# Performance work log

Hardware: AMD Instinct MI355X
Metric: run time of the kernel (lower is better)

The kernel has to match this reference:

```python
import jax, jax.numpy as jnp
import numpy as np

N, E = 50000, 800000
D_IN, HID, H = 128, 64, 4
NEG_SLOPE = 0.2

def setup_inputs() -> dict:
    key = jax.random.key(0)
    ks = jax.random.split(key, 12)
    r = lambda i, shape, s=1.0: jax.random.normal(ks[i], shape, jnp.float32) * s
    return dict(
        x=r(0, (N, D_IN)),
        edge_index=jax.random.randint(ks[1], (2, E), 0, N, jnp.int32),
        W_in=r(2, (D_IN, HID), 0.05), b_in=jnp.zeros((HID,), jnp.float32),
        W1=r(3, (D_IN, H * HID), 0.05), a1_src=r(4, (H, HID), 0.05), a1_dst=r(5, (H, HID), 0.05), b1=jnp.zeros((HID,), jnp.float32),
        W2=r(6, (HID, H * HID), 0.05), a2_src=r(7, (H, HID), 0.05), a2_dst=r(8, (H, HID), 0.05), b2=jnp.zeros((HID,), jnp.float32),
        g1=jnp.ones((HID,), jnp.float32), be1=jnp.zeros((HID,), jnp.float32),
        g2=jnp.ones((HID,), jnp.float32), be2=jnp.zeros((HID,), jnp.float32),
        Wo=r(9, (HID, HID), 0.05), bo=jnp.zeros((HID,), jnp.float32),
    )

def layer_norm(x, g, b, eps=1e-5):
    mu = x.mean(-1, keepdims=True)
    var = ((x - mu) ** 2).mean(-1, keepdims=True)
    return (x - mu) * jax.lax.rsqrt(var + eps) * g + b

def gat_conv(x, W, a_src, a_dst, b, src, dst):
    # PyG GATConv, concat=False (mean over heads), self-loops already in src/dst
    n = x.shape[0]
    h = (x @ W).reshape(n, H, HID)                      # [N,H,C]
    e_src = jnp.einsum('nhc,hc->nh', h, a_src)          # [N,H]
    e_dst = jnp.einsum('nhc,hc->nh', h, a_dst)
    e = jax.nn.leaky_relu(e_src[src] + e_dst[dst], NEG_SLOPE)   # [E+N,H]
    # segment softmax over destination nodes
    m = jax.ops.segment_max(e, dst, num_segments=n)
    e = jnp.exp(e - m[dst])
    s = jax.ops.segment_sum(e, dst, num_segments=n)
    alpha = e / (s[dst] + 1e-16)                        # [E+N,H]
    msg = h[src] * alpha[:, :, None]                    # [E+N,H,C]
    out = jax.ops.segment_sum(msg, dst, num_segments=n) # [N,H,C]
    return out.mean(axis=1) + b                         # concat=False -> mean

def reference(x, W_in, b_in, W1, a1_src, a1_dst, b1, W2, a2_src, a2_dst, b2,
              g1, be1, g2, be2, Wo, bo, edge_index):
    loop = jnp.arange(N, dtype=edge_index.dtype)
    src = jnp.concatenate([edge_index[0], loop])
    dst = jnp.concatenate([edge_index[1], loop])
    residual = x @ W_in + b_in
    h = jax.nn.elu(gat_conv(x, W1, a1_src, a1_dst, b1, src, dst))
    h = layer_norm(h + residual, g1, be1)
    h2 = jax.nn.elu(gat_conv(h, W2, a2_src, a2_dst, b2, src, dst))
    h = layer_norm(h2 + h, g2, be2)
    return h @ Wo + bo
```

## Files before the change

### kernel.cpp

```cpp
#include <hip/hip_runtime.h>


using short8 = __attribute__((ext_vector_type(8))) short;
using floatx4 = __attribute__((ext_vector_type(4))) float;
using floatx2 = __attribute__((ext_vector_type(2))) float;

#define OVCAP 65536

__device__ __forceinline__ float wave_sum(float v) {
#pragma unroll
  for (int m = 32; m >= 1; m >>= 1) v += __shfl_xor(v, m, 64);
  return v;
}
__device__ __forceinline__ float wave_max(float v) {
#pragma unroll
  for (int m = 32; m >= 1; m >>= 1) v = fmaxf(v, __shfl_xor(v, m, 64));
  return v;
}
__device__ __forceinline__ unsigned pack_bf16(float lo, float hi) {
  unsigned r;
  asm volatile("v_cvt_pk_bf16_f32 %0, %1, %2" : "=v"(r) : "v"(lo), "v"(hi));
  return r;
}
__device__ __forceinline__ float bf_lo(unsigned u) { return __uint_as_float(u << 16); }
__device__ __forceinline__ float bf_hi(unsigned u) { return __uint_as_float(u & 0xffff0000u); }
__device__ __forceinline__ float lrelu(float e) { return e > 0.f ? e : 0.2f * e; }
__device__ __forceinline__ unsigned pack_fp8x4(float h0, float h1, float h2,
                                               float h3) {
  int u = __builtin_amdgcn_cvt_pk_fp8_f32(h0, h1, 0, false);
  u = __builtin_amdgcn_cvt_pk_fp8_f32(h2, h3, u, true);
  return (unsigned)u;
}

__device__ __forceinline__ void scatter_edge(const int* __restrict__ src,
                                             const int* __restrict__ dst,
                                             int* __restrict__ cnt,
                                             int* __restrict__ srcs,
                                             uint2* __restrict__ ov,
                                             int* __restrict__ ovcnt, int e) {
  int d = dst[e], s = src[e];
  int pos = atomicAdd(&cnt[d], 1);
  if (pos < 63) {
    srcs[(long)d * 64 + pos] = s;
  } else {
    int o = atomicAdd(ovcnt, 1);
    if (o < OVCAP) ov[o] = make_uint2((unsigned)s, (unsigned)d);
  }
}

__device__ __forceinline__ float waDot(const float* W, const float* a, int k,
                                       int h) {
  float s = 0.f;
#pragma unroll 8
  for (int c = 0; c < 64; ++c) s += W[k * 256 + h * 64 + c] * a[h * 64 + c];
  return s;
}
__device__ __forceinline__ void pack_body(
    int t, int l, const float* __restrict__ W1, const float* __restrict__ Win,
    const float* __restrict__ a1s, const float* __restrict__ a1d,
    const float* __restrict__ W2, const float* __restrict__ a2s,
    const float* __restrict__ a2d, const float* __restrict__ Wo,
    ushort* __restrict__ Bpk1, ushort* __restrict__ Bpk2,
    ushort* __restrict__ Bpk3) {
  const int l15 = l & 15, lhi = l >> 4;
  float w[8];
  ushort* dstp;
  if (t < 84) {
    const int kt = t / 21, nt = t - kt * 21;
    const int kb = kt * 32 + lhi * 8, col = nt * 16 + l15;
#pragma unroll
    for (int e = 0; e < 8; ++e) {
      int k = kb + e;
      float v = 0.f;
      if (col < 256) v = W1[k * 256 + col];
      else if (col < 320) v = Win[k * 64 + (col - 256)];
      else if (col < 324) v = waDot(W1, a1s, k, col - 320);
      else if (col < 328) v = waDot(W1, a1d, k, col - 324);
      w[e] = v;
    }
    dstp = Bpk1 + ((long)t * 64 + l) * 8;
  } else if (t < 120) {
    const int t2 = t - 84;
    if (t2 >= 34) return;
    const int kt = t2 / 17, nt = t2 - kt * 17;
    const int kb = kt * 32 + lhi * 8, col = nt * 16 + l15;
#pragma unroll
    for (int e = 0; e < 8; ++e) {
      int k = kb + e;
      float v = 0.f;
      if (col < 256) v = W2[k * 256 + col];
      else if (col < 260) v = waDot(W2, a2s, k, col - 256);
      else if (col < 264) v = waDot(W2, a2d, k, col - 260);
      w[e] = v;
    }
    dstp = Bpk2 + ((long)t2 * 64 + l) * 8;
  } else {
    const int t3 = t - 120;
    if (t3 >= 8) return;
    const int kt = t3 / 4, nt = t3 - kt * 4;
    const int kb = kt * 32 + lhi * 8, col = nt * 16 + l15;
#pragma unroll
    for (int e = 0; e < 8; ++e) w[e] = Wo[(kb + e) * 64 + col];
    dstp = Bpk3 + ((long)t3 * 64 + l) * 8;
  }
  uint4 o;
  o.x = pack_bf16(w[0], w[1]);
  o.y = pack_bf16(w[2], w[3]);
  o.z = pack_bf16(w[4], w[5]);
  o.w = pack_bf16(w[6], w[7]);
  *(uint4*)dstp = o;
}

template <int KA, int KT, int NT, int MODE>
__device__ __forceinline__ void gemm_body(
    const float* __restrict__ Af32, const ushort* __restrict__ Abf,
    const ushort* __restrict__ Bpk, const float* __restrict__ bias,
    unsigned* __restrict__ Hb, float* __restrict__ eSs,
    float* __restrict__ eDs, float* __restrict__ RES,
    float* __restrict__ outp, int nrows, int bid) {
  const int lane = threadIdx.x & 63;
  const int wid = threadIdx.x >> 6;
  const int row0 = (bid * 4 + wid) * 16;
  if (row0 >= nrows) return;
  const int l15 = lane & 15, lhi = lane >> 4;
  const int rowA = min(row0 + l15, nrows - 1);
  floatx4 acc[NT];
  const floatx4 zero = {0.f, 0.f, 0.f, 0.f};
#pragma unroll
  for (int nt = 0; nt < NT; ++nt) acc[nt] = zero;
#pragma unroll
  for (int kt = 0; kt < KT; ++kt) {
    short8 af;
    if (MODE == 1) {
      const float* ap = Af32 + (long)rowA * KA + lhi * 8 + kt * 32;
      float4 u = *(const float4*)ap;
      float4 v = *(const float4*)(ap + 4);
      union { unsigned u[4]; short8 s; } cv;
      cv.u[0] = pack_bf16(u.x, u.y);
      cv.u[1] = pack_bf16(u.z, u.w);
      cv.u[2] = pack_bf16(v.x, v.y);
      cv.u[3] = pack_bf16(v.z, v.w);
      af = cv.s;
    } else {
      af = *(const short8*)(Abf + (long)rowA * KA + lhi * 8 + kt * 32);
    }
    const ushort* bp = Bpk + ((long)(kt * NT) * 64 + lane) * 8;
#pragma unroll
    for (int nt = 0; nt < NT; ++nt) {
      short8 bf = *(const short8*)(bp + (long)nt * 64 * 8);
      acc[nt] = __builtin_amdgcn_mfma_f32_16x16x32_bf16(af, bf, acc[nt], 0, 0, 0);
    }
  }
#pragma unroll
  for (int reg = 0; reg < 4; ++reg) {
    const int node = row0 + lhi * 4 + reg;
    if (node >= nrows) continue;
    if (MODE == 1 || MODE == 2) {
#pragma unroll
      for (int nt = 0; nt < 4; ++nt) {
        Hb[(long)node * 64 + nt * 16 + l15] =
            pack_fp8x4(acc[nt][reg], acc[nt + 4][reg], acc[nt + 8][reg],
                       acc[nt + 12][reg]);
      }
      if (MODE == 1) {
#pragma unroll
        for (int nt = 16; nt < 20; ++nt) {
          int col = (nt - 16) * 16 + l15;
          RES[(long)node * 64 + col] = acc[nt][reg] + bias[col];
        }
      }
      constexpr int ET = (MODE == 1) ? 20 : 16;
      float ev = acc[ET][reg];
      if (l15 < 4) eSs[node * 4 + l15] = ev;
      else if (l15 < 8) eDs[node * 4 + (l15 - 4)] = ev;
    } else {
#pragma unroll
      for (int nt = 0; nt < NT; ++nt) {
        int col = nt * 16 + l15;
        outp[(long)node * 64 + col] = acc[nt][reg] + bias[col];
      }
    }
  }
}

__global__ __launch_bounds__(256) void pack_scatter_kernel(
    const float* __restrict__ W1, const float* __restrict__ Win,
    const float* __restrict__ a1s, const float* __restrict__ a1d,
    const float* __restrict__ W2, const float* __restrict__ a2s,
    const float* __restrict__ a2d, const float* __restrict__ Wo,
    ushort* __restrict__ Bpk1, ushort* __restrict__ Bpk2,
    ushort* __restrict__ Bpk3, const int* __restrict__ src,
    const int* __restrict__ dst, int* __restrict__ cnt,
    int* __restrict__ srcs, uint2* __restrict__ ov, int* __restrict__ ovcnt,
    int Eh) {
  const int b = blockIdx.x;
  if (b < 32) {
    pack_body(b * 4 + (threadIdx.x >> 6), threadIdx.x & 63, W1, Win, a1s, a1d,
              W2, a2s, a2d, Wo, Bpk1, Bpk2, Bpk3);
    return;
  }
  int e = (b - 32) * 256 + threadIdx.x;
  if (e < Eh) scatter_edge(src, dst, cnt, srcs, ov, ovcnt, e);
}

__global__ __launch_bounds__(256) void gemm1_scatter_kernel(
    const float* __restrict__ Af32, const ushort* __restrict__ Bpk1,
    const float* __restrict__ bias, unsigned* __restrict__ Hb,
    float* __restrict__ eSs, float* __restrict__ eDs, float* __restrict__ RES,
    int nrows, int gemmBlocks, const int* __restrict__ src,
    const int* __restrict__ dst, int* __restrict__ cnt,
    int* __restrict__ srcs, uint2* __restrict__ ov, int* __restrict__ ovcnt,
    int Eh, int E) {
  const int b = blockIdx.x;
  if (b < gemmBlocks) {
    gemm_body<128, 4, 21, 1>(Af32, nullptr, Bpk1, bias, Hb, eSs, eDs, RES,
                             nullptr, nrows, b);
    return;
  }
  int e = Eh + (b - gemmBlocks) * 256 + threadIdx.x;
  if (e < E) scatter_edge(src, dst, cnt, srcs, ov, ovcnt, e);
}

template <int KA, int KT, int NT, int MODE>
__global__ __launch_bounds__(256) void mfma_gemm_kernel(
    const float* __restrict__ Af32, const ushort* __restrict__ Abf,
    const ushort* __restrict__ Bpk, const float* __restrict__ bias,
    unsigned* __restrict__ Hb, float* __restrict__ eSs,
    float* __restrict__ eDs, float* __restrict__ RES,
    float* __restrict__ outp, int nrows) {
  gemm_body<KA, KT, NT, MODE>(Af32, Abf, Bpk, bias, Hb, eSs, eDs, RES, outp,
                              nrows, blockIdx.x);
}

__global__ __launch_bounds__(256) void agg_kernel(
    const int* __restrict__ cnt, const int* __restrict__ srcs,
    const unsigned* __restrict__ Hb, const float4* __restrict__ eS,
    const float4* __restrict__ eD, const float* __restrict__ bias,
    const float* __restrict__ resid, const float* __restrict__ gamma,
    const float* __restrict__ beta, float* __restrict__ out,
    ushort* __restrict__ outbf, const uint2* __restrict__ ov,
    const int* __restrict__ ovcnt, int n) {
  const int lane = threadIdx.x & 63;
  const int node = blockIdx.x * 4 + (threadIdx.x >> 6);
  if (node >= n) return;
  const int deg = cnt[node];
  const int start = node * 64;
  const float4 ed = eD[node];

  float a0 = 0.f, a1 = 0.f, a2 = 0.f, a3 = 0.f;

  if (deg <= 63) {
    const int slot = max(0, min(lane - 1, deg - 1));
    const int sv = srcs[start + slot];
    const int sj = (lane == 0 || lane > deg) ? node : sv;
    const bool act = lane <= deg;
    const float4 es = eS[sj];
    float e0 = lrelu(es.x + ed.x), e1 = lrelu(es.y + ed.y);
    float e2 = lrelu(es.z + ed.z), e3 = lrelu(es.w + ed.w);
    float m0 = wave_max(act ? e0 : -1e30f), m1 = wave_max(act ? e1 : -1e30f);
    float m2 = wave_max(act ? e2 : -1e30f), m3 = wave_max(act ? e3 : -1e30f);
    float p0 = act ? __expf(e0 - m0) : 0.f;
    float p1 = act ? __expf(e1 - m1) : 0.f;
    float p2 = act ? __expf(e2 - m2) : 0.f;
    float p3 = act ? __expf(e3 - m3) : 0.f;
    float s0 = wave_sum(p0), s1 = wave_sum(p1);
    float s2 = wave_sum(p2), s3 = wave_sum(p3);
    p0 *= 1.f / (s0 + 1e-16f);
    p1 *= 1.f / (s1 + 1e-16f);
    p2 *= 1.f / (s2 + 1e-16f);
    p3 *= 1.f / (s3 + 1e-16f);
    const unsigned apk01 = pack_bf16(p0, p1);
    const unsigned apk23 = pack_bf16(p2, p3);

    const unsigned* HbL = Hb + lane;
    const int cntUp = (deg + 4) & ~3;
#define LOADJ(dstv, jj)                                   \
  {                                                       \
    int s_ = __builtin_amdgcn_readlane(sj, (jj));         \
    dstv = HbL[(long)s_ * 64];                            \
  }
#define CONSJ(hv, jj)                                                     \
  {                                                                       \
    unsigned q01 = __builtin_amdgcn_readlane(apk01, (jj));                \
    unsigned q23 = __builtin_amdgcn_readlane(apk23, (jj));                \
    floatx2 l01 = __builtin_amdgcn_cvt_pk_f32_fp8((int)hv, false);        \
    floatx2 l23 = __builtin_amdgcn_cvt_pk_f32_fp8((int)hv, true);         \
    a0 = fmaf(bf_lo(q01), l01.x, a0);                                     \
    a1 = fmaf(bf_hi(q01), l01.y, a1);                                     \
    a2 = fmaf(bf_lo(q23), l23.x, a2);                                     \
    a3 = fmaf(bf_hi(q23), l23.y, a3);                                     \
  }
    unsigned hA, hB, hC, hD;
    LOADJ(hA, 0) LOADJ(hB, 1) LOADJ(hC, 2) LOADJ(hD, 3)
    int j = 0;
    for (; j + 8 <= cntUp; j += 4) {
      unsigned nA, nB, nC, nD;
      LOADJ(nA, j + 4) LOADJ(nB, j + 5) LOADJ(nC, j + 6) LOADJ(nD, j + 7)
      CONSJ(hA, j) CONSJ(hB, j + 1) CONSJ(hC, j + 2) CONSJ(hD, j + 3)
      hA = nA; hB = nB; hC = nC; hD = nD;
    }
    CONSJ(hA, j) CONSJ(hB, j + 1) CONSJ(hC, j + 2) CONSJ(hD, j + 3)
#undef LOADJ
#undef CONSJ
  } else {
    int ovn = min(*ovcnt, OVCAP);
    const int sv = (lane < 63) ? srcs[start + lane] : node;
    float4 es = eS[sv];
    float e0 = lrelu(es.x + ed.x), e1 = lrelu(es.y + ed.y);
    float e2 = lrelu(es.z + ed.z), e3 = lrelu(es.w + ed.w);
    float M0 = e0, M1 = e1, M2 = e2, M3 = e3;
    for (int i = lane; i < ovn; i += 64) {
      uint2 o = ov[i];
      if ((int)o.y == node) {
        float4 eo = eS[o.x];
        M0 = fmaxf(M0, lrelu(eo.x + ed.x));
        M1 = fmaxf(M1, lrelu(eo.y + ed.y));
        M2 = fmaxf(M2, lrelu(eo.z + ed.z));
        M3 = fmaxf(M3, lrelu(eo.w + ed.w));
      }
    }
    float m0 = wave_max(M0), m1 = wave_max(M1);
    float m2 = wave_max(M2), m3 = wave_max(M3);
    float S0 = __expf(e0 - m0), S1 = __expf(e1 - m1);
    float S2 = __expf(e2 - m2), S3 = __expf(e3 - m3);
    for (int i = lane; i < ovn; i += 64) {
      uint2 o = ov[i];
      if ((int)o.y == node) {
        float4 eo = eS[o.x];
        S0 += __expf(lrelu(eo.x + ed.x) - m0);
        S1 += __expf(lrelu(eo.y + ed.y) - m1);
        S2 += __expf(lrelu(eo.z + ed.z) - m2);
        S3 += __expf(lrelu(eo.w + ed.w) - m3);
      }
    }
    float i0 = 1.f / (wave_sum(S0) + 1e-16f), i1 = 1.f / (wave_sum(S1) + 1e-16f);
    float i2 = 1.f / (wave_sum(S2) + 1e-16f), i3 = 1.f / (wave_sum(S3) + 1e-16f);
#define ACCE(sidx)                                                        \
  {                                                                       \
    int s_ = (sidx);                                                      \
    unsigned h = Hb[(long)s_ * 64 + lane];                                \
    float4 e_ = eS[s_];                                                   \
    floatx2 l01 = __builtin_amdgcn_cvt_pk_f32_fp8((int)h, false);         \
    floatx2 l23 = __builtin_amdgcn_cvt_pk_f32_fp8((int)h, true);          \
    float al;                                                             \
    al = __expf(lrelu(e_.x + ed.x) - m0) * i0;                            \
    a0 = fmaf(al, l01.x, a0);                                             \
    al = __expf(lrelu(e_.y + ed.y) - m1) * i1;                            \
    a1 = fmaf(al, l01.y, a1);                                             \
    al = __expf(lrelu(e_.z + ed.z) - m2) * i2;                            \
    a2 = fmaf(al, l23.x, a2);                                             \
    al = __expf(lrelu(e_.w + ed.w) - m3) * i3;                            \
    a3 = fmaf(al, l23.y, a3);                                             \
  }
    for (int i = 0; i < 63; ++i) ACCE(srcs[start + i]);
    ACCE(node);
    for (int k = 0; k < ovn; ++k) {
      uint2 o = ov[k];
      if ((int)o.y == node) ACCE((int)o.x);
    }
#undef ACCE
  }

  float o = (a0 + a1 + a2 + a3) * 0.25f + bias[lane];
  o = o > 0.f ? o : (__expf(o) - 1.f);
  float v = o + resid[(long)node * 64 + lane];
  float mean = wave_sum(v) * (1.f / 64.f);
  float d = v - mean;
  float var = wave_sum(d * d) * (1.f / 64.f);
  float r = rsqrtf(var + 1e-5f);
  float res = d * r * gamma[lane] + beta[lane];
  if (out) out[(long)node * 64 + lane] = res;
  outbf[(long)node * 64 + lane] = (ushort)pack_bf16(res, res);
}

extern "C" void kernel_launch(void* const* d_in, const int* in_sizes, int n_in,
                              void* d_out, int out_size, void* d_ws,
                              size_t ws_size, hipStream_t stream) {
  const float* x    = (const float*)d_in[0];
  const int*   ei   = (const int*)d_in[1];
  const float* W_in = (const float*)d_in[2];
  const float* b_in = (const float*)d_in[3];
  const float* W1   = (const float*)d_in[4];
  const float* a1s  = (const float*)d_in[5];
  const float* a1d  = (const float*)d_in[6];
  const float* b1   = (const float*)d_in[7];
  const float* W2   = (const float*)d_in[8];
  const float* a2s  = (const float*)d_in[9];
  const float* a2d  = (const float*)d_in[10];
  const float* b2   = (const float*)d_in[11];
  const float* g1   = (const float*)d_in[12];
  const float* be1  = (const float*)d_in[13];
  const float* g2   = (const float*)d_in[14];
  const float* be2  = (const float*)d_in[15];
  const float* Wo   = (const float*)d_in[16];
  const float* bo   = (const float*)d_in[17];
  float* out = (float*)d_out;

  const int N = in_sizes[0] / 128;
  const int E = in_sizes[1] / 2;
  const int* src = ei;
  const int* dst = ei + E;

  char* p = (char*)d_ws;
  unsigned* Hb = (unsigned*)p;    p += (long)N * 64 * 4;
  float* RES   = (float*)p;       p += (long)N * 64 * 4;
  float* HL1   = (float*)p;       p += (long)N * 64 * 4;
  ushort* HLbf = (ushort*)p;      p += (long)N * 64 * 2;
  float* eSs   = (float*)p;       p += (long)N * 4 * 4;
  float* eDs   = (float*)p;       p += (long)N * 4 * 4;
  ushort* Bpk1 = (ushort*)p;      p += 84L * 64 * 8 * 2;
  ushort* Bpk2 = (ushort*)p;      p += 34L * 64 * 8 * 2;
  ushort* Bpk3 = (ushort*)p;      p += 8L * 64 * 8 * 2;
  int* cnt     = (int*)p;         p += (long)N * 4;
  int* ovcnt   = (int*)p;         p += 16;
  int* srcs    = (int*)p;         p += (long)N * 64 * 4;
  uint2* ov    = (uint2*)p;       p += (long)OVCAP * 8;

  const dim3 blk(256);
  const int nodeGrid = (N + 3) / 4;
  const int gemmBlocks = (N + 63) / 64;
  const int Eh = E / 2;

  hipMemsetAsync(cnt, 0, (long)N * 4 + 16, stream);

  pack_scatter_kernel<<<32 + (Eh + 255) / 256, blk, 0, stream>>>(
      W1, W_in, a1s, a1d, W2, a2s, a2d, Wo, Bpk1, Bpk2, Bpk3, src, dst, cnt,
      srcs, ov, ovcnt, Eh);
  gemm1_scatter_kernel<<<gemmBlocks + (E - Eh + 255) / 256, blk, 0, stream>>>(
      x, Bpk1, b_in, Hb, eSs, eDs, RES, N, gemmBlocks, src, dst, cnt, srcs,
      ov, ovcnt, Eh, E);

  agg_kernel<<<nodeGrid, blk, 0, stream>>>(
      cnt, srcs, Hb, (const float4*)eSs, (const float4*)eDs, b1, RES, g1, be1,
      HL1, HLbf, ov, ovcnt, N);

  mfma_gemm_kernel<64, 2, 17, 2><<<gemmBlocks, blk, 0, stream>>>(
      nullptr, HLbf, Bpk2, b_in, Hb, eSs, eDs, nullptr, nullptr, N);

  agg_kernel<<<nodeGrid, blk, 0, stream>>>(
      cnt, srcs, Hb, (const float4*)eSs, (const float4*)eDs, b2, HL1, g2, be2,
      nullptr, HLbf, ov, ovcnt, N);

  mfma_gemm_kernel<64, 2, 4, 3><<<gemmBlocks, blk, 0, stream>>>(
      nullptr, HLbf, Bpk3, bo, nullptr, nullptr, nullptr, nullptr, out, N);
}
```

Before: 198.5 us.

## Partition edge scatter by destination range across XCDs and share softmax max

```diff
diff --git a/kernel.cpp b/kernel.cpp
--- a/kernel.cpp
+++ b/kernel.cpp
@@ -32,13 +32,18 @@
   return (unsigned)u;
 }
 
-__device__ __forceinline__ void scatter_edge(const int* __restrict__ src,
-                                             const int* __restrict__ dst,
-                                             int* __restrict__ cnt,
-                                             int* __restrict__ srcs,
-                                             uint2* __restrict__ ov,
-                                             int* __restrict__ ovcnt, int e) {
-  int d = dst[e], s = src[e];
+__device__ __forceinline__ void scatter_chunk(const int* __restrict__ src,
+                                              const int* __restrict__ dst,
+                                              int* __restrict__ cnt,
+                                              int* __restrict__ srcs,
+                                              uint2* __restrict__ ov,
+                                              int* __restrict__ ovcnt, int E,
+                                              int chunk, int part) {
+  int e = chunk * 256 + threadIdx.x;
+  if (e >= E) return;
+  int d = dst[e];
+  if (((d >> 10) & 7) != part) return;
+  int s = src[e];
   int pos = atomicAdd(&cnt[d], 1);
   if (pos < 63) {
     srcs[(long)d * 64 + pos] = s;
@@ -55,13 +60,15 @@
   for (int c = 0; c < 64; ++c) s += W[k * 256 + h * 64 + c] * a[h * 64 + c];
   return s;
 }
-__device__ __forceinline__ void pack_body(
-    int t, int l, const float* __restrict__ W1, const float* __restrict__ Win,
+__global__ __launch_bounds__(256) void pack_kernel(
+    const float* __restrict__ W1, const float* __restrict__ Win,
     const float* __restrict__ a1s, const float* __restrict__ a1d,
     const float* __restrict__ W2, const float* __restrict__ a2s,
     const float* __restrict__ a2d, const float* __restrict__ Wo,
     ushort* __restrict__ Bpk1, ushort* __restrict__ Bpk2,
     ushort* __restrict__ Bpk3) {
+  const int t = blockIdx.x * 4 + (threadIdx.x >> 6);
+  const int l = threadIdx.x & 63;
   const int l15 = l & 15, lhi = l >> 4;
   float w[8];
   ushort* dstp;
@@ -183,26 +190,6 @@
   }
 }
 
-__global__ __launch_bounds__(256) void pack_scatter_kernel(
-    const float* __restrict__ W1, const float* __restrict__ Win,
-    const float* __restrict__ a1s, const float* __restrict__ a1d,
-    const float* __restrict__ W2, const float* __restrict__ a2s,
-    const float* __restrict__ a2d, const float* __restrict__ Wo,
-    ushort* __restrict__ Bpk1, ushort* __restrict__ Bpk2,
-    ushort* __restrict__ Bpk3, const int* __restrict__ src,
-    const int* __restrict__ dst, int* __restrict__ cnt,
-    int* __restrict__ srcs, uint2* __restrict__ ov, int* __restrict__ ovcnt,
-    int Eh) {
-  const int b = blockIdx.x;
-  if (b < 32) {
-    pack_body(b * 4 + (threadIdx.x >> 6), threadIdx.x & 63, W1, Win, a1s, a1d,
-              W2, a2s, a2d, Wo, Bpk1, Bpk2, Bpk3);
-    return;
-  }
-  int e = (b - 32) * 256 + threadIdx.x;
-  if (e < Eh) scatter_edge(src, dst, cnt, srcs, ov, ovcnt, e);
-}
-
 __global__ __launch_bounds__(256) void gemm1_scatter_kernel(
     const float* __restrict__ Af32, const ushort* __restrict__ Bpk1,
     const float* __restrict__ bias, unsigned* __restrict__ Hb,
@@ -210,15 +197,17 @@
     int nrows, int gemmBlocks, const int* __restrict__ src,
     const int* __restrict__ dst, int* __restrict__ cnt,
     int* __restrict__ srcs, uint2* __restrict__ ov, int* __restrict__ ovcnt,
-    int Eh, int E) {
+    int E, int nChunk) {
   const int b = blockIdx.x;
   if (b < gemmBlocks) {
     gemm_body<128, 4, 21, 1>(Af32, nullptr, Bpk1, bias, Hb, eSs, eDs, RES,
                              nullptr, nrows, b);
     return;
   }
-  int e = Eh + (b - gemmBlocks) * 256 + threadIdx.x;
-  if (e < E) scatter_edge(src, dst, cnt, srcs, ov, ovcnt, e);
+  const int sidx = b - gemmBlocks;
+  const int chunk = sidx >> 3;
+  if (chunk >= nChunk) return;
+  scatter_chunk(src, dst, cnt, srcs, ov, ovcnt, E, chunk, b & 7);
 }
 
 template <int KA, int KT, int NT, int MODE>
@@ -257,12 +246,12 @@
     const float4 es = eS[sj];
     float e0 = lrelu(es.x + ed.x), e1 = lrelu(es.y + ed.y);
     float e2 = lrelu(es.z + ed.z), e3 = lrelu(es.w + ed.w);
-    float m0 = wave_max(act ? e0 : -1e30f), m1 = wave_max(act ? e1 : -1e30f);
-    float m2 = wave_max(act ? e2 : -1e30f), m3 = wave_max(act ? e3 : -1e30f);
-    float p0 = act ? __expf(e0 - m0) : 0.f;
-    float p1 = act ? __expf(e1 - m1) : 0.f;
-    float p2 = act ? __expf(e2 - m2) : 0.f;
-    float p3 = act ? __expf(e3 - m3) : 0.f;
+    float em = fmaxf(fmaxf(e0, e1), fmaxf(e2, e3));
+    float M = wave_max(act ? em : -1e30f);
+    float p0 = act ? __expf(e0 - M) : 0.f;
+    float p1 = act ? __expf(e1 - M) : 0.f;
+    float p2 = act ? __expf(e2 - M) : 0.f;
+    float p3 = act ? __expf(e3 - M) : 0.f;
     float s0 = wave_sum(p0), s1 = wave_sum(p1);
     float s2 = wave_sum(p2), s3 = wave_sum(p3);
     p0 *= 1.f / (s0 + 1e-16f);
@@ -272,12 +261,12 @@
     const unsigned apk01 = pack_bf16(p0, p1);
     const unsigned apk23 = pack_bf16(p2, p3);
 
-    const unsigned* HbL = Hb + lane;
     const int cntUp = (deg + 4) & ~3;
 #define LOADJ(dstv, jj)                                   \
   {                                                       \
     int s_ = __builtin_amdgcn_readlane(sj, (jj));         \
-    dstv = HbL[(long)s_ * 64];                            \
+    const unsigned* b_ = Hb + ((size_t)(unsigned)s_ << 6);\
+    dstv = b_[lane];                                      \
   }
 #define CONSJ(hv, jj)                                                     \
   {                                                                       \
@@ -419,16 +408,15 @@
   const dim3 blk(256);
   const int nodeGrid = (N + 3) / 4;
   const int gemmBlocks = (N + 63) / 64;
-  const int Eh = E / 2;
+  const int nChunk = (E + 255) / 256;
 
   hipMemsetAsync(cnt, 0, (long)N * 4 + 16, stream);
 
-  pack_scatter_kernel<<<32 + (Eh + 255) / 256, blk, 0, stream>>>(
-      W1, W_in, a1s, a1d, W2, a2s, a2d, Wo, Bpk1, Bpk2, Bpk3, src, dst, cnt,
-      srcs, ov, ovcnt, Eh);
-  gemm1_scatter_kernel<<<gemmBlocks + (E - Eh + 255) / 256, blk, 0, stream>>>(
+  pack_kernel<<<32, blk, 0, stream>>>(W1, W_in, a1s, a1d, W2, a2s, a2d, Wo,
+                                      Bpk1, Bpk2, Bpk3);
+  gemm1_scatter_kernel<<<gemmBlocks + 8 * nChunk, blk, 0, stream>>>(
       x, Bpk1, b_in, Hb, eSs, eDs, RES, N, gemmBlocks, src, dst, cnt, srcs,
-      ov, ovcnt, Eh, E);
+      ov, ovcnt, E, nChunk);
 
   agg_kernel<<<nodeGrid, blk, 0, stream>>>(
       cnt, srcs, Hb, (const float4*)eSs, (const float4*)eDs, b1, RES, g1, be1,
```

Result: slower. 210.1 us (+5.8%).
